# Optimization experiments

Hardware: AMD Instinct MI355X
Metric: run time of the kernel (lower is better)

The kernel has to match this reference:

```python
import jax, jax.numpy as jnp
import numpy as np

B, C, L = 8, 512, 4096
KC, VC, H = 512, 512, 8
DK, DV = KC // H, VC // H
EPS = 1e-5


def _ln(x, g, b):
    m = jnp.mean(x, axis=-1, keepdims=True)
    v = jnp.var(x, axis=-1, keepdims=True)
    return (x - m) * jax.lax.rsqrt(v + EPS) * g + b


def setup_inputs() -> dict:
    key = jax.random.key(0)
    ks = jax.random.split(key, 12)
    s = 0.02
    return {
        "z1": jax.random.normal(ks[0], (B, C, L), jnp.float32),
        "z2": jax.random.normal(ks[1], (B, C, L), jnp.float32),
        "Wq": jax.random.normal(ks[2], (KC, C), jnp.float32) * s,
        "bq": jnp.zeros((KC,), jnp.float32),
        "Wk": jax.random.normal(ks[3], (KC, C), jnp.float32) * s,
        "bk": jnp.zeros((KC,), jnp.float32),
        "Wv": jax.random.normal(ks[4], (VC, C), jnp.float32) * s,
        "bv": jnp.zeros((VC,), jnp.float32),
        "Wr": jax.random.normal(ks[5], (C, VC), jnp.float32) * s,
        "br": jnp.zeros((C,), jnp.float32),
        "g1": jnp.ones((C,), jnp.float32),
        "be1": jnp.zeros((C,), jnp.float32),
        "W1": jax.random.normal(ks[6], (2 * C, C), jnp.float32) * s,
        "b1": jnp.zeros((2 * C,), jnp.float32),
        "W2": jax.random.normal(ks[7], (C, 2 * C), jnp.float32) * s,
        "b2": jnp.zeros((C,), jnp.float32),
        "g2": jnp.ones((C,), jnp.float32),
        "be2": jnp.zeros((C,), jnp.float32),
    }


def reference(z1, z2, Wq, bq, Wk, bk, Wv, bv, Wr, br, g1, be1, W1, b1, W2, b2, g2, be2):
    # 1x1 Conv1d projections (channels-first)
    q = jnp.einsum('oc,bcl->bol', Wq, z1) + bq[None, :, None]
    k = jnp.einsum('oc,bcl->bol', Wk, z2) + bk[None, :, None]
    v = jnp.einsum('oc,bcl->bol', Wv, z2) + bv[None, :, None]
    qh = q.reshape(B, H, DK, L)
    kh = k.reshape(B, H, DK, L)
    vh = v.reshape(B, H, DV, L)
    # efficient attention: keys softmax over length, queries over channels
    kh = jax.nn.softmax(kh, axis=-1)
    qh = jax.nn.softmax(qh, axis=2)
    ctx = jnp.einsum('bhkl,bhvl->bhkv', kh, vh)          # [B,H,DK,DV]
    att = jnp.einsum('bhkv,bhkl->bhvl', ctx, qh)          # [B,H,DV,L]
    att = att.reshape(B, VC, L)
    z = jnp.einsum('oc,bcl->bol', Wr, att) + br[None, :, None] + z1  # reprojection + residual
    # b c l -> b l c, LayerNorm, FFN, back
    x = z.transpose(0, 2, 1)
    x = _ln(x, g1, be1)
    h = jax.nn.elu(x @ W1.T + b1)
    y = h @ W2.T + b2
    y = _ln(y, g2, be2)
    return y.transpose(0, 2, 1)
```

## Files before the change

kernel.cpp:

```cpp
#include <hip/hip_runtime.h>
#include <math.h>

#define B_   8
#define C_   512
#define L_   4096
#define H_   8
#define DK_  64
#define C2_  1024

typedef unsigned short ushort;
typedef short     bf16x8_t __attribute__((ext_vector_type(8)));
typedef float     f32x4_t  __attribute__((ext_vector_type(4)));
typedef unsigned short u16x8 __attribute__((ext_vector_type(8)));
typedef unsigned short u16x4 __attribute__((ext_vector_type(4)));

__device__ __forceinline__ float bf2f(ushort u) {
    unsigned int x = ((unsigned int)u) << 16;
    float f; __builtin_memcpy(&f, &x, 4); return f;
}
__device__ __forceinline__ ushort f2bf(float f) {
    unsigned int x; __builtin_memcpy(&x, &f, 4);
    x = (x + 0x7FFFu + ((x >> 16) & 1u)) >> 16;
    return (ushort)x;
}

#define GLOAD_LDS16(gp, lp) \
    __builtin_amdgcn_global_load_lds((const __attribute__((address_space(1))) void*)(gp), \
                                     (__attribute__((address_space(3))) void*)(lp), 16, 0, 0)

__global__ __launch_bounds__(256) void transpose_in(const float* __restrict__ in,
                                                    ushort* __restrict__ out)
{
    const int b = blockIdx.z, c0 = blockIdx.y * 64, l0 = blockIdx.x * 64;
    __shared__ float t[64][65];
    const int tid = threadIdx.x;
    {
        const int c = tid >> 4, l4 = (tid & 15) * 4;
        const float* ip = in + ((size_t)b * C_ + c0) * L_ + l0;
#pragma unroll
        for (int cc = c; cc < 64; cc += 16) {
            float4 v = *(const float4*)(ip + (size_t)cc * L_ + l4);
            t[l4 + 0][cc] = v.x; t[l4 + 1][cc] = v.y;
            t[l4 + 2][cc] = v.z; t[l4 + 3][cc] = v.w;
        }
    }
    __syncthreads();
    {
        const int l = tid >> 3, c8 = (tid & 7) * 8;
        ushort* op = out + ((size_t)b * L_ + l0) * C_ + c0;
#pragma unroll
        for (int ll = l; ll < 64; ll += 32) {
            u16x8 v;
#pragma unroll
            for (int i = 0; i < 8; ++i) v[i] = f2bf(t[ll][c8 + i]);
            *(u16x8*)(op + (size_t)ll * C_ + c8) = v;
        }
    }
}

__global__ __launch_bounds__(256) void transpose_out(const float* __restrict__ in,
                                                     float* __restrict__ out)
{
    const int b = blockIdx.z, c0 = blockIdx.y * 64, l0 = blockIdx.x * 64;
    __shared__ float t[64][65];
    const int tid = threadIdx.x;
    {
        const int l = tid >> 4, c4 = (tid & 15) * 4;
#pragma unroll
        for (int ll = l; ll < 64; ll += 16) {
            float4 v = *(const float4*)(in + ((size_t)(b * L_ + l0 + ll)) * C_ + c0 + c4);
            t[c4 + 0][ll] = v.x; t[c4 + 1][ll] = v.y;
            t[c4 + 2][ll] = v.z; t[c4 + 3][ll] = v.w;
        }
    }
    __syncthreads();
    {
        const int c = tid >> 4, l4 = (tid & 15) * 4;
        float* op = out + ((size_t)b * C_ + c0) * L_ + l0;
#pragma unroll
        for (int cc = c; cc < 64; cc += 16) {
            float4 v = {t[cc][l4], t[cc][l4 + 1], t[cc][l4 + 2], t[cc][l4 + 3]};
            *(float4*)(op + (size_t)cc * L_ + l4) = v;
        }
    }
}

__global__ __launch_bounds__(256) void cvt_bf16(const float* __restrict__ in,
                                                ushort* __restrict__ out, int n4)
{
    const int i = blockIdx.x * 256 + threadIdx.x;
    if (i < n4) {
        float4 v = *(const float4*)(in + 4 * (size_t)i);
        u16x4 o; o[0] = f2bf(v.x); o[1] = f2bf(v.y); o[2] = f2bf(v.z); o[3] = f2bf(v.w);
        *(u16x4*)(out + 4 * (size_t)i) = o;
    }
}

__global__ __launch_bounds__(256) void zero_kernel(float* __restrict__ p, int n4)
{
    const int i = blockIdx.x * 256 + threadIdx.x;
    if (i < n4) { float4 z = {0.f, 0.f, 0.f, 0.f}; *(float4*)(p + 4 * (size_t)i) = z; }
}

template<int ACT, bool HAS_RES>
__global__ __launch_bounds__(256) void conv_mfma(
    const ushort* __restrict__ A, const ushort* __restrict__ Wt,
    const float* __restrict__ bias, const ushort* __restrict__ res,
    ushort* __restrict__ out, int M, int N, int K)
{
    const int m0 = blockIdx.x * 128;
    const int n0 = blockIdx.y * 128;
    const int tid = threadIdx.x;
    const int w = tid >> 6, lane = tid & 63;
    const int wm = (w & 1) * 64, wn = (w >> 1) * 64;
    const int l16 = lane & 15, quad = lane >> 4;

    __shared__ ushort sA[128 * 32];
    __shared__ ushort sB[128 * 32];

    f32x4_t acc[4][4];
#pragma unroll
    for (int i = 0; i < 4; ++i)
#pragma unroll
        for (int j = 0; j < 4; ++j) acc[i][j] = (f32x4_t){0.f, 0.f, 0.f, 0.f};

    const int srow = lane >> 2;
    const int sslot = lane & 3;

    for (int c0 = 0; c0 < K; c0 += 32) {
        __syncthreads();
#pragma unroll
        for (int r = 0; r < 2; ++r) {
            const int row = r * 64 + w * 16 + srow;
            const int lk = sslot ^ ((row >> 2) & 3);
            const ushort* ga = A  + (size_t)(m0 + row) * K + c0 + lk * 8;
            const ushort* gb = Wt + (size_t)(n0 + row) * K + c0 + lk * 8;
            ushort* la = sA + (r * 64 + w * 16) * 32;
            ushort* lb = sB + (r * 64 + w * 16) * 32;
            GLOAD_LDS16(ga, la);
            GLOAD_LDS16(gb, lb);
        }
        __syncthreads();

        bf16x8_t af[4], bf[4];
#pragma unroll
        for (int i = 0; i < 4; ++i) {
            const int arow = wm + i * 16 + l16;
            const int ap = quad ^ ((arow >> 2) & 3);
            af[i] = *(const bf16x8_t*)(sA + arow * 32 + ap * 8);
            const int brow = wn + i * 16 + l16;
            const int bp = quad ^ ((brow >> 2) & 3);
            bf[i] = *(const bf16x8_t*)(sB + brow * 32 + bp * 8);
        }
#pragma unroll
        for (int i = 0; i < 4; ++i)
#pragma unroll
            for (int j = 0; j < 4; ++j)
                acc[i][j] = __builtin_amdgcn_mfma_f32_16x16x32_bf16(af[i], bf[j], acc[i][j], 0, 0, 0);
    }

#pragma unroll
    for (int j = 0; j < 4; ++j) {
        const int o = n0 + wn + j * 16 + l16;
        const float bo = bias[o];
#pragma unroll
        for (int i = 0; i < 4; ++i) {
            const int mb = m0 + wm + i * 16 + quad * 4;
#pragma unroll
            for (int r = 0; r < 4; ++r) {
                float t = acc[i][j][r] + bo;
                const size_t idx = (size_t)(mb + r) * N + o;
                if (HAS_RES) t += bf2f(res[idx]);
                if (ACT == 1) t = (t > 0.f) ? t : (__expf(t) - 1.f);
                out[idx] = f2bf(t);
            }
        }
    }
}

__global__ __launch_bounds__(256) void kstat_chunk(const ushort* __restrict__ k,
                                                   float2* __restrict__ stats)
{
    const int cg = blockIdx.x;
    const int bc = blockIdx.y;
    const int b = bc >> 3, ch = bc & 7;
    const int tid = threadIdx.x;
    const int g = tid & 7;
    const int kk = tid >> 3;
    const int w = tid >> 6, lane = tid & 63;
    const ushort* base = k + ((size_t)(b * L_) + ch * 512) * C_ + cg * 64 + g * 8;

    __shared__ float red[4][8][8];
    __shared__ float mcol[64];

    float fm[8];
#pragma unroll
    for (int i = 0; i < 8; ++i) fm[i] = -3.0e38f;
    for (int r = kk; r < 512; r += 32) {
        u16x8 v = *(const u16x8*)(base + (size_t)r * C_);
#pragma unroll
        for (int i = 0; i < 8; ++i) fm[i] = fmaxf(fm[i], bf2f(v[i]));
    }
#pragma unroll
    for (int off = 8; off <= 32; off <<= 1)
#pragma unroll
        for (int i = 0; i < 8; ++i) fm[i] = fmaxf(fm[i], __shfl_xor(fm[i], off));
    if ((lane >> 3) == 0)
#pragma unroll
        for (int i = 0; i < 8; ++i) red[w][g][i] = fm[i];
    __syncthreads();
    if (tid < 64) {
        const int g2 = tid >> 3, j = tid & 7;
        mcol[g2 * 8 + j] = fmaxf(fmaxf(red[0][g2][j], red[1][g2][j]),
                                 fmaxf(red[2][g2][j], red[3][g2][j]));
    }
    __syncthreads();
    float fmc[8];
#pragma unroll
    for (int i = 0; i < 8; ++i) fmc[i] = mcol[g * 8 + i];

    float fs[8] = {};
    for (int r = kk; r < 512; r += 32) {
        u16x8 v = *(const u16x8*)(base + (size_t)r * C_);
#pragma unroll
        for (int i = 0; i < 8; ++i) fs[i] += __expf(bf2f(v[i]) - fmc[i]);
    }
#pragma unroll
    for (int off = 8; off <= 32; off <<= 1)
#pragma unroll
        for (int i = 0; i < 8; ++i) fs[i] += __shfl_xor(fs[i], off);
    __syncthreads();
    if ((lane >> 3) == 0)
#pragma unroll
        for (int i = 0; i < 8; ++i) red[w][g][i] = fs[i];
    __syncthreads();
    if (tid < 64) {
        const int g2 = tid >> 3, j = tid & 7;
        const float s = red[0][g2][j] + red[1][g2][j] + red[2][g2][j] + red[3][g2][j];
        const int c = cg * 64 + g2 * 8 + j;
        stats[((size_t)(b * C_ + c)) * 8 + ch] = make_float2(mcol[g2 * 8 + j], s);
    }
}

__global__ __launch_bounds__(256) void kstat_merge(const float2* __restrict__ stats,
                                                   float2* __restrict__ minv)
{
    const int i = blockIdx.x * 256 + threadIdx.x;
    if (i >= B_ * C_) return;
    float2 st[8];
    float m = -3.0e38f;
#pragma unroll
    for (int ch = 0; ch < 8; ++ch) { st[ch] = stats[(size_t)i * 8 + ch]; m = fmaxf(m, st[ch].x); }
    float s = 0.f;
#pragma unroll
    for (int ch = 0; ch < 8; ++ch) s += st[ch].y * __expf(st[ch].x - m);
    minv[i] = make_float2(m, 1.f / s);
}

__global__ __launch_bounds__(256) void ctx_accum(
    const ushort* __restrict__ kk, const ushort* __restrict__ vv,
    const float2* __restrict__ minv, float* __restrict__ ctx)
{
    const int bh = blockIdx.y, b = bh >> 3, h = bh & 7;
    const int l0 = blockIdx.x * 512;
    const int tid = threadIdx.x;
    __shared__ float sK[32][72];
    __shared__ float sV[32][72];
    const int srow = tid >> 3, c8 = (tid & 7) * 8;
    const int dv4 = (tid & 15) * 4, dk4 = (tid >> 4) * 4;

    float2 cst[8];
    {
        const float2* mp = minv + (size_t)b * C_ + h * 64 + c8;
#pragma unroll
        for (int i = 0; i < 8; ++i) cst[i] = mp[i];
    }
    float acc[4][4] = {};

    for (int lt = 0; lt < 512; lt += 32) {
        const size_t gbase = ((size_t)(b * L_ + l0 + lt + srow)) * C_ + h * 64 + c8;
        u16x8 kv = *(const u16x8*)(kk + gbase);
        u16x8 vvv = *(const u16x8*)(vv + gbase);
        __syncthreads();
#pragma unroll
        for (int i = 0; i < 8; ++i) {
            sK[srow][c8 + i] = __expf(bf2f(kv[i]) - cst[i].x) * cst[i].y;
            sV[srow][c8 + i] = bf2f(vvv[i]);
        }
        __syncthreads();
#pragma unroll
        for (int ll = 0; ll < 32; ++ll) {
            const float4 a = *(const float4*)&sV[ll][dv4];
            const float4 bb = *(const float4*)&sK[ll][dk4];
            const float av[4] = {a.x, a.y, a.z, a.w};
            const float bv[4] = {bb.x, bb.y, bb.z, bb.w};
#pragma unroll
            for (int i = 0; i < 4; ++i)
#pragma unroll
                for (int j = 0; j < 4; ++j)
                    acc[i][j] = fmaf(av[i], bv[j], acc[i][j]);
        }
    }
    float* cp = ctx + (size_t)bh * 4096;
#pragma unroll
    for (int i = 0; i < 4; ++i)
#pragma unroll
        for (int j = 0; j < 4; ++j)
            atomicAdd(&cp[(dv4 + i) * 64 + (dk4 + j)], acc[i][j]);
}

__global__ __launch_bounds__(256) void att_mfma(
    const ushort* __restrict__ q, const float* __restrict__ ctx,
    ushort* __restrict__ att)
{
    const int bh = blockIdx.y, b = bh >> 3, h = bh & 7;
    const int l0 = blockIdx.x * 128;
    const int tid = threadIdx.x, w = tid >> 6, lane = tid & 63;
    const int l16 = lane & 15, quad = lane >> 4;

    __shared__ ushort sQ[128 * 72];
    __shared__ ushort sC[64 * 72];

    {
        const int part = tid & 7;
#pragma unroll
        for (int rr = tid >> 3; rr < 128; rr += 32) {
            u16x8 v = *(const u16x8*)(q + ((size_t)(b * L_ + l0 + rr)) * C_ + h * 64 + part * 8);
            float f[8], m = -3.0e38f;
#pragma unroll
            for (int i = 0; i < 8; ++i) { f[i] = bf2f(v[i]); m = fmaxf(m, f[i]); }
            m = fmaxf(m, __shfl_xor(m, 1));
            m = fmaxf(m, __shfl_xor(m, 2));
            m = fmaxf(m, __shfl_xor(m, 4));
            float s = 0.f;
#pragma unroll
            for (int i = 0; i < 8; ++i) { f[i] = __expf(f[i] - m); s += f[i]; }
            s += __shfl_xor(s, 1); s += __shfl_xor(s, 2); s += __shfl_xor(s, 4);
            const float inv = 1.f / s;
            u16x8 o;
#pragma unroll
            for (int i = 0; i < 8; ++i) o[i] = f2bf(f[i] * inv);
            *(u16x8*)(sQ + rr * 72 + part * 8) = o;
        }
        const int dv = tid >> 2, dk0 = (tid & 3) * 16;
        const float* cp = ctx + (size_t)bh * 4096 + dv * 64 + dk0;
#pragma unroll
        for (int i = 0; i < 16; ++i) sC[dv * 72 + dk0 + i] = f2bf(cp[i]);
    }
    __syncthreads();

    f32x4_t acc[2][4];
#pragma unroll
    for (int i = 0; i < 2; ++i)
#pragma unroll
        for (int j = 0; j < 4; ++j) acc[i][j] = (f32x4_t){0.f, 0.f, 0.f, 0.f};

#pragma unroll
    for (int ks = 0; ks < 2; ++ks) {
        const int k0 = ks * 32;
        bf16x8_t aq[2], bc[4];
#pragma unroll
        for (int i = 0; i < 2; ++i)
            aq[i] = *(const bf16x8_t*)(sQ + (w * 32 + i * 16 + l16) * 72 + k0 + quad * 8);
#pragma unroll
        for (int j = 0; j < 4; ++j)
            bc[j] = *(const bf16x8_t*)(sC + (j * 16 + l16) * 72 + k0 + quad * 8);
#pragma unroll
        for (int i = 0; i < 2; ++i)
#pragma unroll
            for (int j = 0; j < 4; ++j)
                acc[i][j] = __builtin_amdgcn_mfma_f32_16x16x32_bf16(aq[i], bc[j], acc[i][j], 0, 0, 0);
    }

#pragma unroll
    for (int j = 0; j < 4; ++j)
#pragma unroll
        for (int i = 0; i < 2; ++i) {
            const int mb = l0 + w * 32 + i * 16 + quad * 4;
#pragma unroll
            for (int r = 0; r < 4; ++r)
                att[((size_t)(b * L_ + mb + r)) * C_ + h * 64 + j * 16 + l16] = f2bf(acc[i][j][r]);
        }
}

template<bool OUTF32>
__global__ __launch_bounds__(256) void ln_row(
    const ushort* __restrict__ in, const float* __restrict__ g,
    const float* __restrict__ be, ushort* __restrict__ outb,
    float* __restrict__ outf)
{
    const int tid = threadIdx.x, w = tid >> 6, lane = tid & 63;
    const size_t row = (size_t)blockIdx.x * 4 + w;
    const ushort* p = in + row * C_ + lane * 8;
    u16x8 v = *(const u16x8*)p;
    float f[8], s = 0.f, s2 = 0.f;
#pragma unroll
    for (int i = 0; i < 8; ++i) { f[i] = bf2f(v[i]); s += f[i]; s2 = fmaf(f[i], f[i], s2); }
#pragma unroll
    for (int o = 1; o < 64; o <<= 1) { s += __shfl_xor(s, o); s2 += __shfl_xor(s2, o); }
    const float mean = s * (1.f / C_);
    const float var  = s2 * (1.f / C_) - mean * mean;
    const float inv  = rsqrtf(var + 1e-5f);
    if (OUTF32) {
        float* op = outf + row * C_ + lane * 8;
#pragma unroll
        for (int i = 0; i < 8; ++i)
            op[i] = (f[i] - mean) * inv * g[lane * 8 + i] + be[lane * 8 + i];
    } else {
        u16x8 ov;
#pragma unroll
        for (int i = 0; i < 8; ++i)
            ov[i] = f2bf((f[i] - mean) * inv * g[lane * 8 + i] + be[lane * 8 + i]);
        *(u16x8*)(outb + row * C_ + lane * 8) = ov;
    }
}

extern "C" void kernel_launch(void* const* d_in, const int* in_sizes, int n_in,
                              void* d_out, int out_size, void* d_ws, size_t ws_size,
                              hipStream_t stream)
{
    const float* z1  = (const float*)d_in[0];
    const float* z2  = (const float*)d_in[1];
    const float* Wq  = (const float*)d_in[2];
    const float* bq  = (const float*)d_in[3];
    const float* Wk  = (const float*)d_in[4];
    const float* bk  = (const float*)d_in[5];
    const float* Wv  = (const float*)d_in[6];
    const float* bv  = (const float*)d_in[7];
    const float* Wr  = (const float*)d_in[8];
    const float* br  = (const float*)d_in[9];
    const float* g1  = (const float*)d_in[10];
    const float* be1 = (const float*)d_in[11];
    const float* W1  = (const float*)d_in[12];
    const float* b1  = (const float*)d_in[13];
    const float* W2  = (const float*)d_in[14];
    const float* b2  = (const float*)d_in[15];
    const float* g2  = (const float*)d_in[16];
    const float* be2 = (const float*)d_in[17];
    float* out = (float*)d_out;

    const size_t SB = (size_t)B_ * L_ * C_;
    ushort* ws16 = (ushort*)d_ws;
    ushort* b0v = ws16;
    ushort* b1v = ws16 + SB;
    ushort* b2v = ws16 + 2 * SB;
    ushort* b3v = ws16 + 3 * SB;
    ushort* wb  = ws16 + 4 * SB;
    ushort* wbq = wb;
    ushort* wbk = wb + 262144;
    ushort* wbv = wb + 524288;
    ushort* wbr = wb + 786432;
    ushort* wb1 = wb + 1048576;
    ushort* wb2 = wb + 1572864;
    float*  ctxf = (float*)(wb + 2097152);
    float2* stats = (float2*)(ctxf + 65536);
    float2* minv  = stats + (size_t)B_ * C_ * 8;
    ushort* vbuf = (ushort*)d_out;
    ushort* hbuf = (ushort*)d_out;
    float*  yf32 = (float*)b2v;

    const dim3 blk(256);
    const int M = B_ * L_;

    transpose_in<<<dim3(L_/64, C_/64, B_), blk, 0, stream>>>(z1, b0v);
    transpose_in<<<dim3(L_/64, C_/64, B_), blk, 0, stream>>>(z2, b1v);
    cvt_bf16<<<dim3(262144/4/256), blk, 0, stream>>>(Wq, wbq, 262144/4);
    cvt_bf16<<<dim3(262144/4/256), blk, 0, stream>>>(Wk, wbk, 262144/4);
    cvt_bf16<<<dim3(262144/4/256), blk, 0, stream>>>(Wv, wbv, 262144/4);
    cvt_bf16<<<dim3(262144/4/256), blk, 0, stream>>>(Wr, wbr, 262144/4);
    cvt_bf16<<<dim3(524288/4/256), blk, 0, stream>>>(W1, wb1, 524288/4);
    cvt_bf16<<<dim3(524288/4/256), blk, 0, stream>>>(W2, wb2, 524288/4);

    conv_mfma<0,false><<<dim3(M/128, C_/128), blk, 0, stream>>>(b0v, wbq, bq, nullptr, b2v, M, C_, C_);
    conv_mfma<0,false><<<dim3(M/128, C_/128), blk, 0, stream>>>(b1v, wbk, bk, nullptr, b3v, M, C_, C_);
    conv_mfma<0,false><<<dim3(M/128, C_/128), blk, 0, stream>>>(b1v, wbv, bv, nullptr, vbuf, M, C_, C_);

    kstat_chunk<<<dim3(C_/64, B_ * 8), blk, 0, stream>>>(b3v, stats);
    kstat_merge<<<dim3((B_ * C_ + 255) / 256), blk, 0, stream>>>(stats, minv);

    zero_kernel<<<dim3(65536/256), blk, 0, stream>>>(ctxf, 65536);
    ctx_accum<<<dim3(8, B_ * H_), blk, 0, stream>>>(b3v, vbuf, minv, ctxf);

    att_mfma<<<dim3(L_/128, B_ * H_), blk, 0, stream>>>(b2v, ctxf, b1v);

    conv_mfma<0,true><<<dim3(M/128, C_/128), blk, 0, stream>>>(b1v, wbr, br, b0v, b2v, M, C_, C_);

    ln_row<false><<<dim3(M/4), blk, 0, stream>>>(b2v, g1, be1, b3v, nullptr);

    conv_mfma<1,false><<<dim3(M/128, C2_/128), blk, 0, stream>>>(b3v, wb1, b1, nullptr, hbuf, M, C2_, C_);

    conv_mfma<0,false><<<dim3(M/128, C_/128), blk, 0, stream>>>(hbuf, wb2, b2, nullptr, b0v, M, C_, C2_);

    ln_row<true><<<dim3(M/4), blk, 0, stream>>>(b0v, g2, be2, nullptr, yf32);

    transpose_out<<<dim3(L_/64, C_/64, B_), blk, 0, stream>>>(yf32, out);
}
```

Baseline: 602.4 us.

## Double-buffer conv GEMM LDS loads and stage epilogue through LDS for coalesced stores

The conv_mfma GEMM now double-buffers its shared-memory tiles, issuing global-to-LDS loads for the next K slice while MFMAs run on the current one, with one barrier per iteration instead of two. The MFMA operands are swapped so each lane holds four consecutive output columns. The epilogue applies bias, residual and ELU on these vectors, writes them to a per-wave padded LDS tile, then stores 16-byte coalesced rows to global memory instead of scattered 2-byte writes. This roughly doubles LDS use, which may lower occupancy.

Result: faster. 577.7 us (-4.1%).

```diff
diff --git a/kernel.cpp b/kernel.cpp
--- a/kernel.cpp
+++ b/kernel.cpp
@@ -115,8 +115,7 @@
     const int wm = (w & 1) * 64, wn = (w >> 1) * 64;
     const int l16 = lane & 15, quad = lane >> 4;
 
-    __shared__ ushort sA[128 * 32];
-    __shared__ ushort sB[128 * 32];
+    __shared__ ushort smem[18432];
 
     f32x4_t acc[4][4];
 #pragma unroll
@@ -127,53 +126,93 @@
     const int srow = lane >> 2;
     const int sslot = lane & 3;
 
-    for (int c0 = 0; c0 < K; c0 += 32) {
-        __syncthreads();
-#pragma unroll
-        for (int r = 0; r < 2; ++r) {
-            const int row = r * 64 + w * 16 + srow;
-            const int lk = sslot ^ ((row >> 2) & 3);
-            const ushort* ga = A  + (size_t)(m0 + row) * K + c0 + lk * 8;
-            const ushort* gb = Wt + (size_t)(n0 + row) * K + c0 + lk * 8;
-            ushort* la = sA + (r * 64 + w * 16) * 32;
-            ushort* lb = sB + (r * 64 + w * 16) * 32;
-            GLOAD_LDS16(ga, la);
-            GLOAD_LDS16(gb, lb);
-        }
-        __syncthreads();
-
-        bf16x8_t af[4], bf[4];
+    const ushort* gA[2]; const ushort* gB[2];
+    ushort* lA[2]; ushort* lB[2];
+#pragma unroll
+    for (int r = 0; r < 2; ++r) {
+        const int row = r * 64 + w * 16 + srow;
+        const int lk = sslot ^ ((row >> 2) & 3);
+        gA[r] = A  + (size_t)(m0 + row) * K + lk * 8;
+        gB[r] = Wt + (size_t)(n0 + row) * K + lk * 8;
+        lA[r] = smem + (r * 64 + w * 16) * 32;
+        lB[r] = smem + 4096 + (r * 64 + w * 16) * 32;
+    }
+
+    const int nt = K >> 5;
+
+#pragma unroll
+    for (int r = 0; r < 2; ++r) {
+        GLOAD_LDS16(gA[r], lA[r]);
+        GLOAD_LDS16(gB[r], lB[r]);
+    }
+    __syncthreads();
+
+    for (int t = 0; t < nt; ++t) {
+        const int cur = t & 1;
+        if (t + 1 < nt) {
+            const int nb = (cur ^ 1) * 8192;
+            const size_t co = (size_t)(t + 1) * 32;
+#pragma unroll
+            for (int r = 0; r < 2; ++r) {
+                GLOAD_LDS16(gA[r] + co, lA[r] + nb);
+                GLOAD_LDS16(gB[r] + co, lB[r] + nb);
+            }
+        }
+        const ushort* bA = smem + cur * 8192;
+        const ushort* bB = bA + 4096;
+        bf16x8_t amf[4], wf[4];
 #pragma unroll
         for (int i = 0; i < 4; ++i) {
             const int arow = wm + i * 16 + l16;
             const int ap = quad ^ ((arow >> 2) & 3);
-            af[i] = *(const bf16x8_t*)(sA + arow * 32 + ap * 8);
+            amf[i] = *(const bf16x8_t*)(bA + arow * 32 + ap * 8);
             const int brow = wn + i * 16 + l16;
             const int bp = quad ^ ((brow >> 2) & 3);
-            bf[i] = *(const bf16x8_t*)(sB + brow * 32 + bp * 8);
+            wf[i] = *(const bf16x8_t*)(bB + brow * 32 + bp * 8);
         }
 #pragma unroll
         for (int i = 0; i < 4; ++i)
 #pragma unroll
             for (int j = 0; j < 4; ++j)
-                acc[i][j] = __builtin_amdgcn_mfma_f32_16x16x32_bf16(af[i], bf[j], acc[i][j], 0, 0, 0);
-    }
-
+                acc[i][j] = __builtin_amdgcn_mfma_f32_16x16x32_bf16(wf[j], amf[i], acc[i][j], 0, 0, 0);
+        if (t + 1 < nt) __syncthreads();
+    }
+
+    __syncthreads();
+    ushort* sT = smem + w * 4608;
 #pragma unroll
     for (int j = 0; j < 4; ++j) {
-        const int o = n0 + wn + j * 16 + l16;
-        const float bo = bias[o];
+        const int nb = wn + j * 16 + quad * 4;
+        const float4 bo = *(const float4*)(bias + n0 + nb);
+        const float bv[4] = {bo.x, bo.y, bo.z, bo.w};
 #pragma unroll
         for (int i = 0; i < 4; ++i) {
-            const int mb = m0 + wm + i * 16 + quad * 4;
-#pragma unroll
-            for (int r = 0; r < 4; ++r) {
-                float t = acc[i][j][r] + bo;
-                const size_t idx = (size_t)(mb + r) * N + o;
-                if (HAS_RES) t += bf2f(res[idx]);
-                if (ACT == 1) t = (t > 0.f) ? t : (__expf(t) - 1.f);
-                out[idx] = f2bf(t);
+            const int ml = i * 16 + l16;
+            float v[4];
+#pragma unroll
+            for (int r = 0; r < 4; ++r) v[r] = acc[i][j][r] + bv[r];
+            if (HAS_RES) {
+                const u16x4 rv = *(const u16x4*)(res + (size_t)(m0 + wm + ml) * N + n0 + nb);
+#pragma unroll
+                for (int r = 0; r < 4; ++r) v[r] += bf2f(rv[r]);
             }
+            if (ACT == 1) {
+#pragma unroll
+                for (int r = 0; r < 4; ++r) v[r] = (v[r] > 0.f) ? v[r] : (__expf(v[r]) - 1.f);
+            }
+            u16x4 pv;
+#pragma unroll
+            for (int r = 0; r < 4; ++r) pv[r] = f2bf(v[r]);
+            *(u16x4*)(sT + ml * 72 + (nb - wn)) = pv;
+        }
+    }
+    {
+        const int rr = lane >> 3, ch = lane & 7;
+#pragma unroll
+        for (int rep = 0; rep < 8; ++rep) {
+            const int ml = rep * 8 + rr;
+            const u16x8 vo = *(const u16x8*)(sT + ml * 72 + ch * 8);
+            *(u16x8*)(out + (size_t)(m0 + wm + ml) * N + n0 + wn + ch * 8) = vo;
         }
     }
 }
```
